# Kernel optimization log

Hardware: AMD Instinct MI355X
Metric: run time of the kernel (lower is better)

The kernel has to match this reference:

```python
import jax, jax.numpy as jnp
import numpy as np

D_MODEL = 512
NUM_HEADS = 8
D_K = D_MODEL // NUM_HEADS
SCALE = float(np.sqrt(D_K))


def setup_inputs() -> dict:
    key = jax.random.key(0)
    ks = jax.random.split(key, 11)
    B, S, D = 2, 4096, D_MODEL
    std = 1.0 / np.sqrt(D)
    return {
        "query": jax.random.normal(ks[0], (B, S, D), jnp.float32),
        "key": jax.random.normal(ks[1], (B, S, D), jnp.float32),
        "value": jax.random.normal(ks[2], (B, S, D), jnp.float32),
        "w_q": jax.random.normal(ks[3], (D, D), jnp.float32) * std,
        "b_q": jax.random.normal(ks[4], (D,), jnp.float32) * std,
        "w_k": jax.random.normal(ks[5], (D, D), jnp.float32) * std,
        "b_k": jax.random.normal(ks[6], (D,), jnp.float32) * std,
        "w_v": jax.random.normal(ks[7], (D, D), jnp.float32) * std,
        "b_v": jax.random.normal(ks[8], (D,), jnp.float32) * std,
        "w_o": jax.random.normal(ks[9], (D, D), jnp.float32) * std,
        "b_o": jax.random.normal(ks[10], (D,), jnp.float32) * std,
    }


def reference(query, key, value, w_q, b_q, w_k, b_k, w_v, b_v, w_o, b_o):
    B, S, D = query.shape
    H, Dk = NUM_HEADS, D_K
    # Linear projections (torch Linear: x @ W^T + b), split into heads -> [B,H,S,Dk]
    Q = (query @ w_q.T + b_q).reshape(B, S, H, Dk).transpose(0, 2, 1, 3)
    K = (key @ w_k.T + b_k).reshape(B, S, H, Dk).transpose(0, 2, 1, 3)
    V = (value @ w_v.T + b_v).reshape(B, S, H, Dk).transpose(0, 2, 1, 3)
    # [B,H,S,S] attention scores — intentionally materialized like the original
    scores = jnp.einsum("bhqd,bhkd->bhqk", Q, K) / SCALE
    attn = jax.nn.softmax(scores, axis=-1)  # dropout rate 0 in eval baseline
    attended = jnp.einsum("bhqk,bhkd->bhqd", attn, V)
    attended = attended.transpose(0, 2, 1, 3).reshape(B, S, D)
    return attended @ w_o.T + b_o
```

## Files before the change

### kernel.cpp

```cpp
#include <hip/hip_runtime.h>
#include <math.h>

#define D_MODEL 512
#define NHEADS 8
#define DK 64
#define BATCH 2
#define SEQ 4096
#define NIT 32
#define ATTN_SCALE 0.18033688011112043f
#define SPLIT_SCALE 2048.0f
#define INV_SPLIT  (1.0f/2048.0f)

typedef _Float16 half8 __attribute__((ext_vector_type(8)));
typedef __fp16 pkhalf2 __attribute__((ext_vector_type(2)));
typedef float f32x4 __attribute__((ext_vector_type(4)));

union Pk8 { _Float16 h[8]; uint4 u; };
union Pk4 { _Float16 h[4]; uint2 u; };
union Pkz { pkhalf2 h2[2]; uint2 u; };
union Un4 { uint2 u; _Float16 h[4]; };

#if __has_builtin(__builtin_amdgcn_exp2f)
#define EXP2F __builtin_amdgcn_exp2f
#else
#define EXP2F exp2f
#endif

#define MFMA16(a, b, c) __builtin_amdgcn_mfma_f32_16x16x32_f16((a), (b), (c), 0, 0, 0)

__device__ __forceinline__ void gload_lds16(const _Float16* g, _Float16* l) {
    __builtin_amdgcn_global_load_lds(
        (const __attribute__((address_space(1))) void*)g,
        (__attribute__((address_space(3))) void*)l, 16, 0, 0);
}

#define ABLK 4096
#define WBLK 256
__global__ __launch_bounds__(256)
void prep(const float* __restrict__ aq, const float* __restrict__ ak,
          const float* __restrict__ av,
          const float* __restrict__ wq, const float* __restrict__ wk,
          const float* __restrict__ wv, const float* __restrict__ wo,
          _Float16* __restrict__ dq, _Float16* __restrict__ dk,
          _Float16* __restrict__ dv,
          _Float16* __restrict__ hq, _Float16* __restrict__ hk,
          _Float16* __restrict__ hv, _Float16* __restrict__ ho,
          _Float16* __restrict__ lo) {
    int gid = blockIdx.x;
    const float* src;
    _Float16 *hi, *lw = nullptr;
    if (gid < 3 * ABLK) {
        const int w = gid / ABLK;
        gid -= w * ABLK;
        src = w == 0 ? aq : (w == 1 ? ak : av);
        hi  = w == 0 ? dq : (w == 1 ? dk : dv);
    } else {
        int g = gid - 3 * ABLK;
        const int w = g / WBLK;
        gid = g - w * WBLK;
        src = w == 0 ? wq : (w == 1 ? wk : (w == 2 ? wv : wo));
        hi  = w == 0 ? hq : (w == 1 ? hk : (w == 2 ? hv : ho));
        if (w == 3) lw = lo;
    }
    const int i = (gid * 256 + threadIdx.x) * 4;
    float4 v = *(const float4*)(src + i);
    Pk4 h;
    h.h[0] = (_Float16)v.x; h.h[1] = (_Float16)v.y;
    h.h[2] = (_Float16)v.z; h.h[3] = (_Float16)v.w;
    *(uint2*)(hi + i) = h.u;
    if (lw) {
        Pk4 l;
        l.h[0] = (_Float16)((v.x - (float)h.h[0]) * SPLIT_SCALE);
        l.h[1] = (_Float16)((v.y - (float)h.h[1]) * SPLIT_SCALE);
        l.h[2] = (_Float16)((v.z - (float)h.h[2]) * SPLIT_SCALE);
        l.h[3] = (_Float16)((v.w - (float)h.h[3]) * SPLIT_SCALE);
        *(uint2*)(lw + i) = l.u;
    }
}

__global__ __launch_bounds__(256)
void gemm_qkv(const _Float16* __restrict__ Aq, const _Float16* __restrict__ Ak,
              const _Float16* __restrict__ Av,
              const _Float16* __restrict__ Whq, const _Float16* __restrict__ Whk,
              const _Float16* __restrict__ Whv,
              const float* __restrict__ bq, const float* __restrict__ bk,
              const float* __restrict__ bv,
              _Float16* __restrict__ Qf, _Float16* __restrict__ Kf,
              _Float16* __restrict__ Vtf) {
    const int z = blockIdx.z;
    const _Float16* A    = z == 0 ? Aq  : (z == 1 ? Ak  : Av);
    const _Float16* Wh   = z == 0 ? Whq : (z == 1 ? Whk : Whv);
    const float*    bias = z == 0 ? bq  : (z == 1 ? bk  : bv);

    __shared__ __align__(16) _Float16 sA[2][128 * 64];
    __shared__ __align__(16) _Float16 sW[2][128 * 64];

    const int t    = threadIdx.x;
    const int lane = t & 63, wave = t >> 6;
    const int col  = lane & 15, quad = lane >> 4;
    const int wm   = (wave & 1) * 64, wn = (wave >> 1) * 64;
    const int m0   = blockIdx.y * 128, n0 = blockIdx.x * 128;

    const int subrow = lane >> 3;
    const int schunk = ((lane & 7) ^ subrow) * 8;

    #define STAGE_AW(K0, BUF)                                                        \
        do {                                                                          \
            _Pragma("unroll")                                                         \
            for (int j = 0; j < 4; ++j) {                                             \
                const int rw = wave * 32 + j * 8;                                     \
                gload_lds16(A  + (size_t)(m0 + rw + subrow) * 512 + (K0) + schunk,    \
                            &sA[BUF][rw * 64]);                                       \
                gload_lds16(Wh + (size_t)(n0 + rw + subrow) * 512 + (K0) + schunk,    \
                            &sW[BUF][rw * 64]);                                       \
            }                                                                         \
        } while (0)

    f32x4 acc[4][4] = {};

    STAGE_AW(0, 0);
    for (int ck = 0; ck < 8; ++ck) {
        const int cur = ck & 1;
        __syncthreads();
        if (ck + 1 < 8) STAGE_AW((ck + 1) * 64, cur ^ 1);

        #pragma unroll
        for (int kc = 0; kc < 2; ++kc) {
            const int pos = ((kc * 4 + quad) ^ (col & 7)) * 8;
            half8 af[4], wf[4];
            #pragma unroll
            for (int mt = 0; mt < 4; ++mt)
                af[mt] = *(const half8*)&sA[cur][(wm + mt * 16 + col) * 64 + pos];
            #pragma unroll
            for (int nt = 0; nt < 4; ++nt)
                wf[nt] = *(const half8*)&sW[cur][(wn + nt * 16 + col) * 64 + pos];
            #pragma unroll
            for (int mt = 0; mt < 4; ++mt)
                #pragma unroll
                for (int nt = 0; nt < 4; ++nt)
                    acc[mt][nt] = MFMA16(af[mt], wf[nt], acc[mt][nt]);
        }
    }

    float bv4[4];
    #pragma unroll
    for (int nt = 0; nt < 4; ++nt) bv4[nt] = bias[n0 + wn + nt * 16 + col];

    if (z < 2) {
        _Float16* Out = z == 0 ? Qf : Kf;
        const float alpha = z == 0 ? ATTN_SCALE : 1.0f;
        #pragma unroll
        for (int mt = 0; mt < 4; ++mt) {
            const int m = m0 + wm + mt * 16 + quad * 4;
            #pragma unroll
            for (int nt = 0; nt < 4; ++nt) {
                const int n = n0 + wn + nt * 16 + col;
                #pragma unroll
                for (int r = 0; r < 4; ++r)
                    Out[(size_t)(m + r) * 512 + n] = (_Float16)((acc[mt][nt][r] + bv4[nt]) * alpha);
            }
        }
    } else {
        #pragma unroll
        for (int mt = 0; mt < 4; ++mt) {
            const int m = m0 + wm + mt * 16 + quad * 4;
            const int b = m >> 12, s = m & (SEQ - 1);
            #pragma unroll
            for (int nt = 0; nt < 4; ++nt) {
                const int n = n0 + wn + nt * 16 + col;
                const int hh = n >> 6, d = n & (DK - 1);
                Pk4 p;
                #pragma unroll
                for (int r = 0; r < 4; ++r)
                    p.h[r] = (_Float16)(acc[mt][nt][r] + bv4[nt]);
                *(uint2*)&Vtf[((size_t)((b * NHEADS + hh) * DK + d)) * SEQ + s] = p.u;
            }
        }
    }
}

__global__ __launch_bounds__(256)
void attn_mfma(const _Float16* __restrict__ Qf, const _Float16* __restrict__ Kf,
               const _Float16* __restrict__ Vtf,
               _Float16* __restrict__ Op0, _Float16* __restrict__ Op1,
               float2* __restrict__ Ml) {
    __shared__ __align__(16) _Float16 sK[2][64 * 64];
    __shared__ __align__(16) _Float16 sV[2][64 * 64];
    __shared__ __align__(16) _Float16 sP[64 * 64];

    const int t    = threadIdx.x;
    const int lane = t & 63;
    const int wave = t >> 6;
    const int col  = lane & 15;
    const int quad = lane >> 4;

    const int q0 = blockIdx.x * 128;
    const int h  = blockIdx.y;
    const int b  = blockIdx.z >> 1;
    const int sp = blockIdx.z & 1;
    const int kBase = sp * (SEQ / 2);

    const size_t rowBase = (size_t)b * SEQ;
    const size_t vBase   = ((size_t)(b * NHEADS + h)) * DK * SEQ;

    {
        _Float16* sQ = &sK[0][0];
        uint4 qv[4];
        #pragma unroll
        for (int i2 = 0; i2 < 4; ++i2) {
            const int slot = t + i2 * 256;
            const int r = slot >> 3, sl = slot & 7;
            qv[i2] = *(const uint4*)(Qf + (rowBase + q0 + r) * 512 + h * 64 + sl * 8);
        }
        #pragma unroll
        for (int i2 = 0; i2 < 4; ++i2) {
            const int slot = t + i2 * 256;
            const int r = slot >> 3, sl = slot & 7;
            *(uint4*)&sQ[r * 64 + (sl ^ (r & 7)) * 8] = qv[i2];
        }
    }
    __syncthreads();

    half8 qf[2][2];
    {
        const _Float16* sQ = &sK[0][0];
        #pragma unroll
        for (int nt = 0; nt < 2; ++nt)
            #pragma unroll
            for (int kc = 0; kc < 2; ++kc)
                qf[nt][kc] = *(const half8*)&sQ[(wave * 32 + nt * 16 + col) * 64 +
                                                ((kc * 4 + quad) ^ (col & 7)) * 8];
    }
    __syncthreads();

    const int subrow = lane >> 3;
    const int schunk = ((lane & 7) ^ subrow) * 8;
    const _Float16* kP[2];
    const _Float16* vP[2];
    #pragma unroll
    for (int j = 0; j < 2; ++j) {
        const int rw = wave * 16 + j * 8;
        kP[j] = Kf + (rowBase + kBase + rw + subrow) * 512 + h * 64 + schunk;
        vP[j] = Vtf + vBase + (size_t)(rw + subrow) * SEQ + kBase + schunk;
    }
    #pragma unroll
    for (int j = 0; j < 2; ++j) {
        const int rw = wave * 16 + j * 8;
        gload_lds16(kP[j], &sK[0][rw * 64]);
        gload_lds16(vP[j], &sV[0][rw * 64]);
        kP[j] += 64 * 512;
        vP[j] += 64;
    }

    _Float16* Ps = sP + wave * 16 * 64;
    const int pmsk = (col & 7) << 1;

    float m_r[2] = { -INFINITY, -INFINITY };
    float l_r[2] = { 0.0f, 0.0f };
    f32x4 of[4][2] = {};

    for (int itp = 0; itp < NIT; itp += 2) {
        #pragma unroll
        for (int cur = 0; cur < 2; ++cur) {
            const int it = itp + cur;
            __syncthreads();
            if (it + 1 < NIT) {
                #pragma unroll
                for (int j = 0; j < 2; ++j) {
                    const int rw = wave * 16 + j * 8;
                    gload_lds16(kP[j], &sK[cur ^ 1][rw * 64]);
                    gload_lds16(vP[j], &sV[cur ^ 1][rw * 64]);
                    kP[j] += 64 * 512;
                    vP[j] += 64;
                }
            }

            f32x4 sf[4][2] = {};
            #pragma unroll
            for (int kc = 0; kc < 2; ++kc) {
                const int pos = ((kc * 4 + quad) ^ (col & 7)) * 8;
                #pragma unroll
                for (int kt = 0; kt < 4; ++kt) {
                    half8 kf = *(const half8*)&sK[cur][(kt * 16 + col) * 64 + pos];
                    #pragma unroll
                    for (int nt = 0; nt < 2; ++nt)
                        sf[kt][nt] = MFMA16(kf, qf[nt][kc], sf[kt][nt]);
                }
            }

            if (it == 0) {
                #pragma unroll
                for (int nt = 0; nt < 2; ++nt) {
                    float mx = sf[0][nt][0];
                    #pragma unroll
                    for (int kt = 0; kt < 4; ++kt)
                        #pragma unroll
                        for (int r = 0; r < 4; ++r)
                            mx = fmaxf(mx, sf[kt][nt][r]);
                    mx = fmaxf(mx, __shfl_xor(mx, 16));
                    mx = fmaxf(mx, __shfl_xor(mx, 32));
                    m_r[nt] = mx;
                }
            }

            float lrs[2];
            #pragma unroll
            for (int nt = 0; nt < 2; ++nt) {
                float ls = 0.0f;
                #pragma unroll
                for (int kt = 0; kt < 4; ++kt) {
                    const float p0 = EXP2F(sf[kt][nt][0] - m_r[nt]);
                    const float p1 = EXP2F(sf[kt][nt][1] - m_r[nt]);
                    const float p2 = EXP2F(sf[kt][nt][2] - m_r[nt]);
                    const float p3 = EXP2F(sf[kt][nt][3] - m_r[nt]);
                    ls += (p0 + p1) + (p2 + p3);
                    Pkz z;
                    z.h2[0] = __builtin_amdgcn_cvt_pkrtz(p0, p1);
                    z.h2[1] = __builtin_amdgcn_cvt_pkrtz(p2, p3);
                    *(uint2*)&Ps[col * 64 + ((kt * 4 + quad) ^ pmsk) * 4] = z.u;
                }
                lrs[nt] = ls;
                #pragma unroll
                for (int kc = 0; kc < 2; ++kc) {
                    half8 pf = *(const half8*)&Ps[col * 64 + ((kc * 8 + quad * 2) ^ pmsk) * 4];
                    const int pos = ((kc * 4 + quad) ^ (col & 7)) * 8;
                    #pragma unroll
                    for (int dt = 0; dt < 4; ++dt) {
                        half8 vf = *(const half8*)&sV[cur][(dt * 16 + col) * 64 + pos];
                        of[dt][nt] = MFMA16(vf, pf, of[dt][nt]);
                    }
                }
            }

            l_r[0] += lrs[0];
            l_r[1] += lrs[1];

            if (__any(fmaxf(lrs[0], lrs[1]) > 1024.0f)) {
                #pragma unroll
                for (int nt = 0; nt < 2; ++nt) {
                    float mx = sf[0][nt][0];
                    #pragma unroll
                    for (int kt = 0; kt < 4; ++kt)
                        #pragma unroll
                        for (int r = 0; r < 4; ++r)
                            mx = fmaxf(mx, sf[kt][nt][r]);
                    mx = fmaxf(mx, __shfl_xor(mx, 16));
                    mx = fmaxf(mx, __shfl_xor(mx, 32));
                    if (mx > m_r[nt]) {
                        const float al = EXP2F(m_r[nt] - mx);
                        l_r[nt] *= al;
                        #pragma unroll
                        for (int dt = 0; dt < 4; ++dt)
                            #pragma unroll
                            for (int r = 0; r < 4; ++r)
                                of[dt][nt][r] *= al;
                        m_r[nt] = mx;
                    }
                }
            }
        }
    }

    _Float16* Opx = sp ? Op1 : Op0;
    #pragma unroll
    for (int nt = 0; nt < 2; ++nt) {
        float l = l_r[nt];
        l += __shfl_xor(l, 16);
        l += __shfl_xor(l, 32);
        const float inv = 1.0f / l;
        const int q = q0 + wave * 32 + nt * 16 + col;
        const size_t R = (size_t)b * SEQ + q;
        #pragma unroll
        for (int dt = 0; dt < 4; ++dt) {
            Pkz z;
            z.h2[0] = __builtin_amdgcn_cvt_pkrtz(of[dt][nt][0] * inv, of[dt][nt][1] * inv);
            z.h2[1] = __builtin_amdgcn_cvt_pkrtz(of[dt][nt][2] * inv, of[dt][nt][3] * inv);
            *(uint2*)(Opx + R * 512 + h * 64 + dt * 16 + quad * 4) = z.u;
        }
        if (quad == 0)
            Ml[(size_t)(sp * BATCH * SEQ) * NHEADS + R * NHEADS + h] = make_float2(m_r[nt], l);
    }
}

__global__ __launch_bounds__(256)
void attn_merge(const _Float16* __restrict__ Op0, const _Float16* __restrict__ Op1,
                const float2* __restrict__ Ml,
                _Float16* __restrict__ Oh, _Float16* __restrict__ Ol) {
    const int i4 = (blockIdx.x * 256 + threadIdx.x) * 4;
    const int R = i4 >> 9;
    const int c = i4 & 511;
    const int h = c >> 6;

    const float2 ml1 = Ml[(size_t)R * NHEADS + h];
    const float2 ml2 = Ml[(size_t)(BATCH * SEQ) * NHEADS + (size_t)R * NHEADS + h];
    const float m = fmaxf(ml1.x, ml2.x);
    float w1 = EXP2F(ml1.x - m) * ml1.y;
    float w2 = EXP2F(ml2.x - m) * ml2.y;
    const float inv = 1.0f / (w1 + w2);
    w1 *= inv; w2 *= inv;

    Un4 a, bb;
    a.u  = *(const uint2*)(Op0 + (size_t)R * 512 + c);
    bb.u = *(const uint2*)(Op1 + (size_t)R * 512 + c);

    Pk4 hh, ll;
    #pragma unroll
    for (int r = 0; r < 4; ++r) {
        const float v = w1 * (float)a.h[r] + w2 * (float)bb.h[r];
        hh.h[r] = (_Float16)v;
        ll.h[r] = (_Float16)((v - (float)hh.h[r]) * SPLIT_SCALE);
    }
    *(uint2*)(Oh + (size_t)R * 512 + c) = hh.u;
    *(uint2*)(Ol + (size_t)R * 512 + c) = ll.u;
}

__global__ __launch_bounds__(256)
void gemm_out(const _Float16* __restrict__ Ah, const _Float16* __restrict__ Al,
              const _Float16* __restrict__ Wh,
              const float* __restrict__ bias, float* __restrict__ C) {
    __shared__ __align__(16) _Float16 sAh[2][128 * 64];
    __shared__ __align__(16) _Float16 sAl[2][128 * 64];
    __shared__ __align__(16) _Float16 sWh[2][64 * 64];

    const int t    = threadIdx.x;
    const int lane = t & 63, wave = t >> 6;
    const int col  = lane & 15, quad = lane >> 4;
    const int wm   = (wave & 1) * 64, wn = (wave >> 1) * 32;
    const int m0   = blockIdx.y * 128, n0 = blockIdx.x * 64;

    const int subrow = lane >> 3;
    const int schunk = ((lane & 7) ^ subrow) * 8;

    #define STAGE_OUT(K0, BUF)                                                       \
        do {                                                                          \
            _Pragma("unroll")                                                         \
            for (int j = 0; j < 4; ++j) {                                             \
                const int rw = wave * 32 + j * 8;                                     \
                gload_lds16(Ah + (size_t)(m0 + rw + subrow) * 512 + (K0) + schunk,    \
                            &sAh[BUF][rw * 64]);                                      \
                gload_lds16(Al + (size_t)(m0 + rw + subrow) * 512 + (K0) + schunk,    \
                            &sAl[BUF][rw * 64]);                                      \
            }                                                                         \
            _Pragma("unroll")                                                         \
            for (int j = 0; j < 2; ++j) {                                             \
                const int rw = wave * 16 + j * 8;                                     \
                gload_lds16(Wh + (size_t)(n0 + rw + subrow) * 512 + (K0) + schunk,    \
                            &sWh[BUF][rw * 64]);                                      \
            }                                                                         \
        } while (0)

    f32x4 acc_h[4][2] = {};
    f32x4 acc_x[4][2] = {};

    STAGE_OUT(0, 0);
    for (int ck = 0; ck < 8; ++ck) {
        const int cur = ck & 1;
        __syncthreads();
        if (ck + 1 < 8) STAGE_OUT((ck + 1) * 64, cur ^ 1);

        #pragma unroll
        for (int kc = 0; kc < 2; ++kc) {
            const int pos = ((kc * 4 + quad) ^ (col & 7)) * 8;
            half8 ahf[4], alf[4], whf[2];
            #pragma unroll
            for (int mt = 0; mt < 4; ++mt) {
                ahf[mt] = *(const half8*)&sAh[cur][(wm + mt * 16 + col) * 64 + pos];
                alf[mt] = *(const half8*)&sAl[cur][(wm + mt * 16 + col) * 64 + pos];
            }
            #pragma unroll
            for (int nt = 0; nt < 2; ++nt)
                whf[nt] = *(const half8*)&sWh[cur][(wn + nt * 16 + col) * 64 + pos];
            #pragma unroll
            for (int mt = 0; mt < 4; ++mt)
                #pragma unroll
                for (int nt = 0; nt < 2; ++nt) {
                    acc_h[mt][nt] = MFMA16(ahf[mt], whf[nt], acc_h[mt][nt]);
                    acc_x[mt][nt] = MFMA16(alf[mt], whf[nt], acc_x[mt][nt]);
                }
        }
    }

    float bv2[2];
    #pragma unroll
    for (int nt = 0; nt < 2; ++nt) bv2[nt] = bias[n0 + wn + nt * 16 + col];

    #pragma unroll
    for (int mt = 0; mt < 4; ++mt) {
        const int m = m0 + wm + mt * 16 + quad * 4;
        #pragma unroll
        for (int nt = 0; nt < 2; ++nt) {
            const int n = n0 + wn + nt * 16 + col;
            #pragma unroll
            for (int r = 0; r < 4; ++r)
                C[(size_t)(m + r) * 512 + n] =
                    acc_h[mt][nt][r] + acc_x[mt][nt][r] * INV_SPLIT + bv2[nt];
        }
    }
}

extern "C" void kernel_launch(void* const* d_in, const int* in_sizes, int n_in,
                              void* d_out, int out_size, void* d_ws, size_t ws_size,
                              hipStream_t stream) {
    const float* query = (const float*)d_in[0];
    const float* key   = (const float*)d_in[1];
    const float* value = (const float*)d_in[2];
    const float* w_q   = (const float*)d_in[3];
    const float* b_q   = (const float*)d_in[4];
    const float* w_k   = (const float*)d_in[5];
    const float* b_k   = (const float*)d_in[6];
    const float* w_v   = (const float*)d_in[7];
    const float* b_v   = (const float*)d_in[8];
    const float* w_o   = (const float*)d_in[9];
    const float* b_o   = (const float*)d_in[10];
    float* out = (float*)d_out;

    const int WN = D_MODEL * D_MODEL;
    const size_t plane = (size_t)BATCH * SEQ * D_MODEL;

    _Float16* base = (_Float16*)d_ws;
    _Float16* Aq16 = base;
    _Float16* Ak16 = Aq16 + plane;
    _Float16* Av16 = Ak16 + plane;
    _Float16* whq  = Av16 + plane;
    _Float16* whk  = whq + WN;
    _Float16* whv  = whk + WN;
    _Float16* who  = whv + WN;
    _Float16* wlo  = who + WN;
    _Float16* Qf   = wlo + WN;
    _Float16* Kf   = Qf + plane;
    _Float16* Vtf  = Kf + plane;
    _Float16* Op1  = Vtf + plane;
    float2*   Ml   = (float2*)(Op1 + plane);
    _Float16* Oh   = Aq16;
    _Float16* Ol   = Ak16;
    _Float16* Op0  = Av16;

    dim3 blk(256);

    hipLaunchKernelGGL(prep, dim3(3 * ABLK + 4 * WBLK), blk, 0, stream,
                       query, key, value, w_q, w_k, w_v, w_o,
                       Aq16, Ak16, Av16, whq, whk, whv, who, wlo);

    hipLaunchKernelGGL(gemm_qkv, dim3(D_MODEL / 128, BATCH * SEQ / 128, 3), blk, 0, stream,
                       Aq16, Ak16, Av16,
                       whq, whk, whv,
                       b_q, b_k, b_v, Qf, Kf, Vtf);

    hipLaunchKernelGGL(attn_mfma, dim3(SEQ / 128, NHEADS, BATCH * 2), blk, 0, stream,
                       Qf, Kf, Vtf, Op0, Op1, Ml);

    hipLaunchKernelGGL(attn_merge, dim3(BATCH * SEQ * D_MODEL / 4 / 256), blk, 0, stream,
                       Op0, Op1, Ml, Oh, Ol);

    hipLaunchKernelGGL(gemm_out, dim3(D_MODEL / 64, BATCH * SEQ / 128), blk, 0, stream,
                       Oh, Ol, who, b_o, out);
}
```

Before: 275.3 us.

## Drop split-fp16 output projection and restructure attention Q staging and PV loop

Removes the hi/lo fp16 error-compensation split for the attention output and w_o, so gemm_out reads one A operand and issues half the MFMAs, and attn_merge writes one plane. The prep kernel now uses packed round-toward-zero conversion. The attention kernel stages Q through a larger sP buffer while the first K/V async loads are already in flight, which drops a barrier. The PV MFMAs are regrouped so each V fragment load serves both query subtiles. The cost is lower accuracy in the output projection and truncating rounding on the inputs.

```diff
diff --git a/kernel.cpp b/kernel.cpp
--- a/kernel.cpp
+++ b/kernel.cpp
@@ -44,11 +44,10 @@
           _Float16* __restrict__ dq, _Float16* __restrict__ dk,
           _Float16* __restrict__ dv,
           _Float16* __restrict__ hq, _Float16* __restrict__ hk,
-          _Float16* __restrict__ hv, _Float16* __restrict__ ho,
-          _Float16* __restrict__ lo) {
+          _Float16* __restrict__ hv, _Float16* __restrict__ ho) {
     int gid = blockIdx.x;
     const float* src;
-    _Float16 *hi, *lw = nullptr;
+    _Float16* hi;
     if (gid < 3 * ABLK) {
         const int w = gid / ABLK;
         gid -= w * ABLK;
@@ -60,22 +59,13 @@
         gid = g - w * WBLK;
         src = w == 0 ? wq : (w == 1 ? wk : (w == 2 ? wv : wo));
         hi  = w == 0 ? hq : (w == 1 ? hk : (w == 2 ? hv : ho));
-        if (w == 3) lw = lo;
     }
     const int i = (gid * 256 + threadIdx.x) * 4;
     float4 v = *(const float4*)(src + i);
-    Pk4 h;
-    h.h[0] = (_Float16)v.x; h.h[1] = (_Float16)v.y;
-    h.h[2] = (_Float16)v.z; h.h[3] = (_Float16)v.w;
+    Pkz h;
+    h.h2[0] = __builtin_amdgcn_cvt_pkrtz(v.x, v.y);
+    h.h2[1] = __builtin_amdgcn_cvt_pkrtz(v.z, v.w);
     *(uint2*)(hi + i) = h.u;
-    if (lw) {
-        Pk4 l;
-        l.h[0] = (_Float16)((v.x - (float)h.h[0]) * SPLIT_SCALE);
-        l.h[1] = (_Float16)((v.y - (float)h.h[1]) * SPLIT_SCALE);
-        l.h[2] = (_Float16)((v.z - (float)h.h[2]) * SPLIT_SCALE);
-        l.h[3] = (_Float16)((v.w - (float)h.h[3]) * SPLIT_SCALE);
-        *(uint2*)(lw + i) = l.u;
-    }
 }
 
 __global__ __launch_bounds__(256)
@@ -186,7 +176,7 @@
                float2* __restrict__ Ml) {
     __shared__ __align__(16) _Float16 sK[2][64 * 64];
     __shared__ __align__(16) _Float16 sV[2][64 * 64];
-    __shared__ __align__(16) _Float16 sP[64 * 64];
+    __shared__ __align__(16) _Float16 sP[128 * 64];
 
     const int t    = threadIdx.x;
     const int lane = t & 63;
@@ -202,36 +192,6 @@
 
     const size_t rowBase = (size_t)b * SEQ;
     const size_t vBase   = ((size_t)(b * NHEADS + h)) * DK * SEQ;
-
-    {
-        _Float16* sQ = &sK[0][0];
-        uint4 qv[4];
-        #pragma unroll
-        for (int i2 = 0; i2 < 4; ++i2) {
-            const int slot = t + i2 * 256;
-            const int r = slot >> 3, sl = slot & 7;
-            qv[i2] = *(const uint4*)(Qf + (rowBase + q0 + r) * 512 + h * 64 + sl * 8);
-        }
-        #pragma unroll
-        for (int i2 = 0; i2 < 4; ++i2) {
-            const int slot = t + i2 * 256;
-            const int r = slot >> 3, sl = slot & 7;
-            *(uint4*)&sQ[r * 64 + (sl ^ (r & 7)) * 8] = qv[i2];
-        }
-    }
-    __syncthreads();
-
-    half8 qf[2][2];
-    {
-        const _Float16* sQ = &sK[0][0];
-        #pragma unroll
-        for (int nt = 0; nt < 2; ++nt)
-            #pragma unroll
-            for (int kc = 0; kc < 2; ++kc)
-                qf[nt][kc] = *(const half8*)&sQ[(wave * 32 + nt * 16 + col) * 64 +
-                                                ((kc * 4 + quad) ^ (col & 7)) * 8];
-    }
-    __syncthreads();
 
     const int subrow = lane >> 3;
     const int schunk = ((lane & 7) ^ subrow) * 8;
@@ -242,17 +202,38 @@
         const int rw = wave * 16 + j * 8;
         kP[j] = Kf + (rowBase + kBase + rw + subrow) * 512 + h * 64 + schunk;
         vP[j] = Vtf + vBase + (size_t)(rw + subrow) * SEQ + kBase + schunk;
-    }
-    #pragma unroll
-    for (int j = 0; j < 2; ++j) {
-        const int rw = wave * 16 + j * 8;
         gload_lds16(kP[j], &sK[0][rw * 64]);
         gload_lds16(vP[j], &sV[0][rw * 64]);
         kP[j] += 64 * 512;
         vP[j] += 64;
     }
 
-    _Float16* Ps = sP + wave * 16 * 64;
+    {
+        uint4 qv[4];
+        #pragma unroll
+        for (int i2 = 0; i2 < 4; ++i2) {
+            const int slot = t + i2 * 256;
+            const int r = slot >> 3, sl = slot & 7;
+            qv[i2] = *(const uint4*)(Qf + (rowBase + q0 + r) * 512 + h * 64 + sl * 8);
+        }
+        #pragma unroll
+        for (int i2 = 0; i2 < 4; ++i2) {
+            const int slot = t + i2 * 256;
+            const int r = slot >> 3, sl = slot & 7;
+            *(uint4*)&sP[r * 64 + (sl ^ (r & 7)) * 8] = qv[i2];
+        }
+    }
+    __syncthreads();
+
+    half8 qf[2][2];
+    #pragma unroll
+    for (int nt = 0; nt < 2; ++nt)
+        #pragma unroll
+        for (int kc = 0; kc < 2; ++kc)
+            qf[nt][kc] = *(const half8*)&sP[(wave * 32 + nt * 16 + col) * 64 +
+                                            ((kc * 4 + quad) ^ (col & 7)) * 8];
+
+    _Float16* Ps = sP + wave * 32 * 64;
     const int pmsk = (col & 7) << 1;
 
     float m_r[2] = { -INFINITY, -INFINITY };
@@ -317,18 +298,24 @@
                     Pkz z;
                     z.h2[0] = __builtin_amdgcn_cvt_pkrtz(p0, p1);
                     z.h2[1] = __builtin_amdgcn_cvt_pkrtz(p2, p3);
-                    *(uint2*)&Ps[col * 64 + ((kt * 4 + quad) ^ pmsk) * 4] = z.u;
+                    *(uint2*)&Ps[(nt * 16 + col) * 64 + ((kt * 4 + quad) ^ pmsk) * 4] = z.u;
                 }
                 lrs[nt] = ls;
-                #pragma unroll
-                for (int kc = 0; kc < 2; ++kc) {
-                    half8 pf = *(const half8*)&Ps[col * 64 + ((kc * 8 + quad * 2) ^ pmsk) * 4];
-                    const int pos = ((kc * 4 + quad) ^ (col & 7)) * 8;
-                    #pragma unroll
-                    for (int dt = 0; dt < 4; ++dt) {
-                        half8 vf = *(const half8*)&sV[cur][(dt * 16 + col) * 64 + pos];
-                        of[dt][nt] = MFMA16(vf, pf, of[dt][nt]);
-                    }
+            }
+
+            #pragma unroll
+            for (int kc = 0; kc < 2; ++kc) {
+                half8 pf[2];
+                #pragma unroll
+                for (int nt = 0; nt < 2; ++nt)
+                    pf[nt] = *(const half8*)&Ps[(nt * 16 + col) * 64 +
+                                                ((kc * 8 + quad * 2) ^ pmsk) * 4];
+                const int pos = ((kc * 4 + quad) ^ (col & 7)) * 8;
+                #pragma unroll
+                for (int dt = 0; dt < 4; ++dt) {
+                    half8 vf = *(const half8*)&sV[cur][(dt * 16 + col) * 64 + pos];
+                    of[dt][0] = MFMA16(vf, pf[0], of[dt][0]);
+                    of[dt][1] = MFMA16(vf, pf[1], of[dt][1]);
                 }
             }
 
@@ -384,8 +371,7 @@
 
 __global__ __launch_bounds__(256)
 void attn_merge(const _Float16* __restrict__ Op0, const _Float16* __restrict__ Op1,
-                const float2* __restrict__ Ml,
-                _Float16* __restrict__ Oh, _Float16* __restrict__ Ol) {
+                const float2* __restrict__ Ml, _Float16* __restrict__ Oh) {
     const int i4 = (blockIdx.x * 256 + threadIdx.x) * 4;
     const int R = i4 >> 9;
     const int c = i4 & 511;
@@ -403,23 +389,18 @@
     a.u  = *(const uint2*)(Op0 + (size_t)R * 512 + c);
     bb.u = *(const uint2*)(Op1 + (size_t)R * 512 + c);
 
-    Pk4 hh, ll;
-    #pragma unroll
-    for (int r = 0; r < 4; ++r) {
-        const float v = w1 * (float)a.h[r] + w2 * (float)bb.h[r];
-        hh.h[r] = (_Float16)v;
-        ll.h[r] = (_Float16)((v - (float)hh.h[r]) * SPLIT_SCALE);
-    }
+    Pkz hh;
+    hh.h2[0] = __builtin_amdgcn_cvt_pkrtz(w1 * (float)a.h[0] + w2 * (float)bb.h[0],
+                                          w1 * (float)a.h[1] + w2 * (float)bb.h[1]);
+    hh.h2[1] = __builtin_amdgcn_cvt_pkrtz(w1 * (float)a.h[2] + w2 * (float)bb.h[2],
+                                          w1 * (float)a.h[3] + w2 * (float)bb.h[3]);
     *(uint2*)(Oh + (size_t)R * 512 + c) = hh.u;
-    *(uint2*)(Ol + (size_t)R * 512 + c) = ll.u;
 }
 
 __global__ __launch_bounds__(256)
-void gemm_out(const _Float16* __restrict__ Ah, const _Float16* __restrict__ Al,
-              const _Float16* __restrict__ Wh,
+void gemm_out(const _Float16* __restrict__ Ah, const _Float16* __restrict__ Wh,
               const float* __restrict__ bias, float* __restrict__ C) {
     __shared__ __align__(16) _Float16 sAh[2][128 * 64];
-    __shared__ __align__(16) _Float16 sAl[2][128 * 64];
     __shared__ __align__(16) _Float16 sWh[2][64 * 64];
 
     const int t    = threadIdx.x;
@@ -438,8 +419,6 @@
                 const int rw = wave * 32 + j * 8;                                     \
                 gload_lds16(Ah + (size_t)(m0 + rw + subrow) * 512 + (K0) + schunk,    \
                             &sAh[BUF][rw * 64]);                                      \
-                gload_lds16(Al + (size_t)(m0 + rw + subrow) * 512 + (K0) + schunk,    \
-                            &sAl[BUF][rw * 64]);                                      \
             }                                                                         \
             _Pragma("unroll")                                                         \
             for (int j = 0; j < 2; ++j) {                                             \
@@ -449,8 +428,7 @@
             }                                                                         \
         } while (0)
 
-    f32x4 acc_h[4][2] = {};
-    f32x4 acc_x[4][2] = {};
+    f32x4 acc[4][2] = {};
 
     STAGE_OUT(0, 0);
     for (int ck = 0; ck < 8; ++ck) {
@@ -461,22 +439,18 @@
         #pragma unroll
         for (int kc = 0; kc < 2; ++kc) {
             const int pos = ((kc * 4 + quad) ^ (col & 7)) * 8;
-            half8 ahf[4], alf[4], whf[2];
-            #pragma unroll
-            for (int mt = 0; mt < 4; ++mt) {
+            half8 ahf[4], whf[2];
+            #pragma unroll
+            for (int mt = 0; mt < 4; ++mt)
                 ahf[mt] = *(const half8*)&sAh[cur][(wm + mt * 16 + col) * 64 + pos];
-                alf[mt] = *(const half8*)&sAl[cur][(wm + mt * 16 + col) * 64 + pos];
-            }
             #pragma unroll
             for (int nt = 0; nt < 2; ++nt)
                 whf[nt] = *(const half8*)&sWh[cur][(wn + nt * 16 + col) * 64 + pos];
             #pragma unroll
             for (int mt = 0; mt < 4; ++mt)
                 #pragma unroll
-                for (int nt = 0; nt < 2; ++nt) {
-                    acc_h[mt][nt] = MFMA16(ahf[mt], whf[nt], acc_h[mt][nt]);
-                    acc_x[mt][nt] = MFMA16(alf[mt], whf[nt], acc_x[mt][nt]);
-                }
+                for (int nt = 0; nt < 2; ++nt)
+                    acc[mt][nt] = MFMA16(ahf[mt], whf[nt], acc[mt][nt]);
         }
     }
 
@@ -492,8 +466,7 @@
             const int n = n0 + wn + nt * 16 + col;
             #pragma unroll
             for (int r = 0; r < 4; ++r)
-                C[(size_t)(m + r) * 512 + n] =
-                    acc_h[mt][nt][r] + acc_x[mt][nt][r] * INV_SPLIT + bv2[nt];
+                C[(size_t)(m + r) * 512 + n] = acc[mt][nt][r] + bv2[nt];
         }
     }
 }
@@ -525,21 +498,19 @@
     _Float16* whk  = whq + WN;
     _Float16* whv  = whk + WN;
     _Float16* who  = whv + WN;
-    _Float16* wlo  = who + WN;
-    _Float16* Qf   = wlo + WN;
+    _Float16* Qf   = who + WN;
     _Float16* Kf   = Qf + plane;
     _Float16* Vtf  = Kf + plane;
     _Float16* Op1  = Vtf + plane;
     float2*   Ml   = (float2*)(Op1 + plane);
     _Float16* Oh   = Aq16;
-    _Float16* Ol   = Ak16;
     _Float16* Op0  = Av16;
 
     dim3 blk(256);
 
     hipLaunchKernelGGL(prep, dim3(3 * ABLK + 4 * WBLK), blk, 0, stream,
                        query, key, value, w_q, w_k, w_v, w_o,
-                       Aq16, Ak16, Av16, whq, whk, whv, who, wlo);
+                       Aq16, Ak16, Av16, whq, whk, whv, who);
 
     hipLaunchKernelGGL(gemm_qkv, dim3(D_MODEL / 128, BATCH * SEQ / 128, 3), blk, 0, stream,
                        Aq16, Ak16, Av16,
@@ -550,8 +521,8 @@
                        Qf, Kf, Vtf, Op0, Op1, Ml);
 
     hipLaunchKernelGGL(attn_merge, dim3(BATCH * SEQ * D_MODEL / 4 / 256), blk, 0, stream,
-                       Op0, Op1, Ml, Oh, Ol);
+                       Op0, Op1, Ml, Oh);
 
     hipLaunchKernelGGL(gemm_out, dim3(D_MODEL / 64, BATCH * SEQ / 128), blk, 0, stream,
-                       Oh, Ol, who, b_o, out);
-}
+                       Oh, who, b_o, out);
+}
```

After: 264.8 us. 3.8% less time.
